# Kernel optimization log

Hardware: AMD Instinct MI355X
Metric: run time of the kernel (lower is better)

Reference implementation:

```python
import jax, jax.numpy as jnp
import numpy as np

COMMITMENT_COST = 0.25


def setup_inputs() -> dict:
    key = jax.random.key(0)
    k1, k2 = jax.random.split(key)
    x = jax.random.normal(k1, (32, 1024, 512), dtype=jnp.float32)
    codebook = jax.random.normal(k2, (8192, 512), dtype=jnp.float32)
    return {"x": x, "codebook": codebook}


def reference(x, codebook):
    D = codebook.shape[1]
    flat = x.reshape(-1, D)                                   # [N, D]
    # squared L2 distances: ||f||^2 + ||c||^2 - 2 f c^T
    distances = (
        jnp.sum(flat * flat, axis=1, keepdims=True)
        + jnp.sum(codebook * codebook, axis=1)
        - 2.0 * jnp.matmul(flat, codebook.T)                   # [N, K]
    )
    encoding_indices = jnp.argmin(distances, axis=1)           # [N]
    quantized = codebook[encoding_indices].reshape(x.shape)    # [.., D]
    commitment_loss = COMMITMENT_COST * jnp.mean(
        (jax.lax.stop_gradient(quantized) - x) ** 2
    )
    # straight-through estimator
    quantized_st = x + jax.lax.stop_gradient(quantized - x)
    return (quantized_st, commitment_loss)
```

## Files before the change

kernel.cpp:

```cpp
#include <hip/hip_runtime.h>
#include <stdint.h>

#define N_TOT 32768
#define DDIM  512
#define KCB   8192
#define NSPLIT 4
#define COLS_SPLIT (KCB / NSPLIT)
#define BN 128
#define BC 128
#define BKD 64
#define NTILES (COLS_SPLIT / BC)
#define NSTEPS (NTILES * 8)
#define MARGIN 0.15f

#define RB3 32
#define RP3 32
#define RSLOTS (RGRID3 / RP3)
#define RGRID3 2048

typedef _Float16 half8 __attribute__((ext_vector_type(8)));
typedef float    floatx4 __attribute__((ext_vector_type(4)));

typedef const __attribute__((address_space(1))) unsigned int* gas_ptr;
typedef __attribute__((address_space(3))) unsigned int* las_ptr;
__device__ __forceinline__ void gld_lds16(void* l, const void* g) {
    __builtin_amdgcn_global_load_lds((gas_ptr)g, (las_ptr)l, 16, 0, 0);
}

__device__ __forceinline__ unsigned long long shfl_xor_u64(unsigned long long v, int m) {
    unsigned int lo = (unsigned int)v, hi = (unsigned int)(v >> 32);
    lo = __shfl_xor(lo, m, 64);
    hi = __shfl_xor(hi, m, 64);
    return ((unsigned long long)hi << 32) | lo;
}

__global__ __launch_bounds__(256) void convert_x_kernel(
    const float* __restrict__ x, _Float16* __restrict__ xh) {
    size_t i = ((size_t)blockIdx.x * 256 + threadIdx.x) * 8;
    float4 v0 = *(const float4*)(x + i);
    float4 v1 = *(const float4*)(x + i + 4);
    half8 h;
    h[0] = (_Float16)v0.x; h[1] = (_Float16)v0.y; h[2] = (_Float16)v0.z; h[3] = (_Float16)v0.w;
    h[4] = (_Float16)v1.x; h[5] = (_Float16)v1.y; h[6] = (_Float16)v1.z; h[7] = (_Float16)v1.w;
    *(half8*)(xh + i) = h;
}

__global__ __launch_bounds__(256) void convert_cb_kernel(
    const float* __restrict__ cb, _Float16* __restrict__ cbh, float* __restrict__ cnorm) {
    int row = blockIdx.x * 4 + (threadIdx.x >> 6);
    int lane = threadIdx.x & 63;
    const float* src = cb + (size_t)row * DDIM + lane * 8;
    float4 v0 = *(const float4*)src;
    float4 v1 = *(const float4*)(src + 4);
    half8 h;
    h[0] = (_Float16)v0.x; h[1] = (_Float16)v0.y; h[2] = (_Float16)v0.z; h[3] = (_Float16)v0.w;
    h[4] = (_Float16)v1.x; h[5] = (_Float16)v1.y; h[6] = (_Float16)v1.z; h[7] = (_Float16)v1.w;
    *(half8*)(cbh + (size_t)row * DDIM + lane * 8) = h;
    float s = v0.x*v0.x + v0.y*v0.y + v0.z*v0.z + v0.w*v0.w
            + v1.x*v1.x + v1.y*v1.y + v1.z*v1.z + v1.w*v1.w;
#pragma unroll
    for (int off = 32; off > 0; off >>= 1) s += __shfl_down(s, off, 64);
    if (lane == 0) cnorm[row] = s;
}

__global__ __launch_bounds__(256, 2) void gemm_argmin_kernel(
    const _Float16* __restrict__ xh, const _Float16* __restrict__ cbh,
    const float* __restrict__ cnorm,
    float* __restrict__ sb1, int* __restrict__ si1, float* __restrict__ sb2) {

    __shared__ __align__(16) _Float16 smem[32768];
    char* smemb = (char*)smem;

    const int tid = threadIdx.x;
    const int wave = tid >> 6;
    const int lane = tid & 63;
    const int rowHalf = wave >> 1;
    const int colHalf = wave & 1;
    const int l15 = lane & 15;
    const int quad = lane >> 4;

    const int orig = blockIdx.x;
    const int wg = ((orig & 7) << 7) | (orig >> 3);
    const int bx = wg & 255;
    const int by = wg >> 8;
    const int row0 = bx * BN;
    const int colBase = by * COLS_SPLIT;

    int voff[4];
#pragma unroll
    for (int r = 0; r < 4; ++r) {
        int c = wave * 256 + r * 64 + lane;
        int ar = c >> 3;
        int q  = (c & 7) ^ (ar & 7);
        voff[r] = (ar << 9) + q * 8;
    }
    const _Float16* aptr = xh + ((size_t)row0 << 9);
    const _Float16* bptr = cbh + ((size_t)colBase << 9);

    int aaddr[2][4], baddr[2][4];
#pragma unroll
    for (int kh = 0; kh < 2; ++kh) {
#pragma unroll
        for (int i = 0; i < 4; ++i) {
            int rr = rowHalf * 64 + i * 16 + l15;
            int qa = (kh * 4 + quad) ^ (rr & 7);
            aaddr[kh][i] = (rr * 64 + qa * 8) * 2;
            int cc = colHalf * 64 + i * 16 + l15;
            int qb = (kh * 4 + quad) ^ (cc & 7);
            baddr[kh][i] = 16384 + (cc * 64 + qb * 8) * 2;
        }
    }

    float b1[16], b2[16];
    int   i1[16];
#pragma unroll
    for (int s = 0; s < 16; ++s) { b1[s] = 3.402823466e38f; b2[s] = 3.402823466e38f; i1[s] = 0; }

#define STAGE(parv, boffu, d0v) do {                                            \
        _Float16* Asb = smem + (parv) * 16384;                                  \
        _Float16* Bsb = Asb + 8192;                                             \
        _Pragma("unroll")                                                       \
        for (int r = 0; r < 4; ++r) {                                           \
            gld_lds16(Asb + (wave * 256 + r * 64) * 8,                          \
                      aptr + (d0v) + voff[r]);                                  \
            gld_lds16(Bsb + (wave * 256 + r * 64) * 8,                          \
                      bptr + (boffu) + (d0v) + voff[r]);                        \
        }                                                                       \
    } while (0)

    floatx4 acc[4][4];
#pragma unroll
    for (int i = 0; i < 4; ++i)
#pragma unroll
        for (int j = 0; j < 4; ++j)
            acc[i][j] = (floatx4){0.f, 0.f, 0.f, 0.f};

    STAGE(0, 0, 0);
    __syncthreads();

    for (int s = 0; s < NSTEPS; ++s) {
        if (s + 1 < NSTEPS) {
            STAGE((s + 1) & 1, ((s + 1) >> 3) << 16, ((s + 1) & 7) * BKD);
        }
#pragma unroll
        for (int kh = 0; kh < 2; ++kh) {
            half8 af[4], bf[4];
#pragma unroll
            for (int i = 0; i < 4; ++i)
                af[i] = *(const half8*)(smemb + aaddr[kh][i]);
#pragma unroll
            for (int j = 0; j < 4; ++j)
                bf[j] = *(const half8*)(smemb + baddr[kh][j]);
#pragma unroll
            for (int i = 0; i < 4; ++i)
#pragma unroll
                for (int j = 0; j < 4; ++j)
                    acc[i][j] = __builtin_amdgcn_mfma_f32_16x16x32_f16(
                        af[i], bf[j], acc[i][j], 0, 0, 0);
        }
        if ((s & 7) == 7) {
            const int col0 = colBase + (s >> 3) * BC;
#pragma unroll
            for (int j = 0; j < 4; ++j) {
                int col = col0 + colHalf * 64 + j * 16 + l15;
                float cn = cnorm[col];
#pragma unroll
                for (int i = 0; i < 4; ++i) {
#pragma unroll
                    for (int r = 0; r < 4; ++r) {
                        float sc = fmaf(-2.0f, acc[i][j][r], cn);
                        int slot = i * 4 + r;
                        if (sc < b1[slot]) { b2[slot] = b1[slot]; b1[slot] = sc; i1[slot] = col; }
                        else if (sc < b2[slot]) b2[slot] = sc;
                    }
                }
            }
#pragma unroll
            for (int i = 0; i < 4; ++i)
#pragma unroll
                for (int j = 0; j < 4; ++j)
                    acc[i][j] = (floatx4){0.f, 0.f, 0.f, 0.f};
        }
#pragma unroll
        for (int kh = 0; kh < 2; ++kh)
#pragma unroll
            for (int i = 0; i < 4; ++i) { aaddr[kh][i] ^= 32768; baddr[kh][i] ^= 32768; }
        __syncthreads();
    }
#undef STAGE

#pragma unroll
    for (int m = 1; m < 16; m <<= 1) {
#pragma unroll
        for (int s = 0; s < 16; ++s) {
            float ob1 = __shfl_xor(b1[s], m, 64);
            float ob2 = __shfl_xor(b2[s], m, 64);
            int   oi1 = __shfl_xor(i1[s], m, 64);
            if (ob1 < b1[s] || (ob1 == b1[s] && oi1 < i1[s])) {
                b2[s] = fminf(b1[s], ob2);
                b1[s] = ob1; i1[s] = oi1;
            } else {
                b2[s] = fminf(b2[s], ob1);
            }
        }
    }

    float* mb1 = (float*)smem;
    float* mb2 = mb1 + 256;
    int*   mi1 = (int*)(mb2 + 256);
    if (l15 == 0) {
#pragma unroll
        for (int s = 0; s < 16; ++s) {
            int row = rowHalf * 64 + (s >> 2) * 16 + quad * 4 + (s & 3);
            mb1[colHalf * 128 + row] = b1[s];
            mb2[colHalf * 128 + row] = b2[s];
            mi1[colHalf * 128 + row] = i1[s];
        }
    }
    __syncthreads();
    if (tid < 128) {
        float a1 = mb1[tid], a2 = mb2[tid]; int ai = mi1[tid];
        float c1 = mb1[128 + tid], c2 = mb2[128 + tid]; int ci = mi1[128 + tid];
        float r1, r2; int ri;
        if (c1 < a1 || (c1 == a1 && ci < ai)) { r1 = c1; ri = ci; r2 = fminf(a1, c2); }
        else { r1 = a1; ri = ai; r2 = fminf(a2, c1); }
        size_t o = (size_t)by * N_TOT + row0 + tid;
        sb1[o] = r1; si1[o] = ri; sb2[o] = r2;
    }
}

__global__ __launch_bounds__(256) void merge_kernel(
    const float* __restrict__ sb1, const int* __restrict__ si1, const float* __restrict__ sb2,
    int* __restrict__ indices, int* __restrict__ flags,
    int* __restrict__ list, int* __restrict__ count,
    unsigned long long* __restrict__ result) {
    int n = blockIdx.x * 256 + threadIdx.x;
    float b1 = sb1[n]; int i1 = si1[n]; float b2 = sb2[n];
#pragma unroll
    for (int s = 1; s < NSPLIT; ++s) {
        float ob1 = sb1[(size_t)s * N_TOT + n];
        int   oi1 = si1[(size_t)s * N_TOT + n];
        float ob2 = sb2[(size_t)s * N_TOT + n];
        if (ob1 < b1 || (ob1 == b1 && oi1 < i1)) { b2 = fminf(b1, ob2); b1 = ob1; i1 = oi1; }
        else b2 = fminf(b2, ob1);
    }
    indices[n] = i1;
    result[n] = 0xFFFFFFFFFFFFFFFFull;
    int f = (b2 - b1 < MARGIN) ? 1 : 0;
    flags[n] = f;
    if (f) { int pos = atomicAdd(count, 1); list[pos] = n; }
}

__global__ __launch_bounds__(256) void repair3_kernel(
    const float* __restrict__ x, const float* __restrict__ cb,
    const float* __restrict__ cnorm, const int* __restrict__ list,
    const int* __restrict__ count, unsigned long long* __restrict__ result) {
    __shared__ __align__(16) float xs[RB3][512];
    __shared__ unsigned long long red[RB3][4];
    const int tid = threadIdx.x;
    const int lane = tid & 63;
    const int wv = tid >> 6;
    const int part = blockIdx.x & (RP3 - 1);
    const int slot0 = blockIdx.x >> 5;
    const int cnt = *count;
    const int nbatch = (cnt + RB3 - 1) / RB3;
    const int k = part * 256 + tid;
    const float cn = cnorm[k];
    const float* crow = cb + (size_t)k * 512;

    for (int batch = slot0; batch < nbatch; batch += RSLOTS) {
        const int rb = min(RB3, cnt - batch * RB3);
        __syncthreads();
        for (int t = tid; t < rb * 128; t += 256) {
            int b = t >> 7, d4 = t & 127;
            int n = list[batch * RB3 + b];
            ((float4*)xs[b])[d4] = ((const float4*)(x + ((size_t)n << 9)))[d4];
        }
        __syncthreads();

        float d0[RB3], d1[RB3], d2[RB3], d3[RB3];
#pragma unroll
        for (int b = 0; b < RB3; ++b) { d0[b] = 0.f; d1[b] = 0.f; d2[b] = 0.f; d3[b] = 0.f; }

        for (int t = 0; t < 512; t += 16) {
            float4 c0 = *(const float4*)(crow + t);
            float4 c1 = *(const float4*)(crow + t + 4);
            float4 c2 = *(const float4*)(crow + t + 8);
            float4 c3 = *(const float4*)(crow + t + 12);
#pragma unroll
            for (int b = 0; b < RB3; ++b) {
                float4 x0 = *(const float4*)&xs[b][t];
                float4 x1 = *(const float4*)&xs[b][t + 4];
                float4 x2 = *(const float4*)&xs[b][t + 8];
                float4 x3 = *(const float4*)&xs[b][t + 12];
                d0[b] = fmaf(c0.x, x0.x, d0[b]);  d0[b] = fmaf(c0.y, x0.y, d0[b]);
                d0[b] = fmaf(c0.z, x0.z, d0[b]);  d0[b] = fmaf(c0.w, x0.w, d0[b]);
                d1[b] = fmaf(c1.x, x1.x, d1[b]);  d1[b] = fmaf(c1.y, x1.y, d1[b]);
                d1[b] = fmaf(c1.z, x1.z, d1[b]);  d1[b] = fmaf(c1.w, x1.w, d1[b]);
                d2[b] = fmaf(c2.x, x2.x, d2[b]);  d2[b] = fmaf(c2.y, x2.y, d2[b]);
                d2[b] = fmaf(c2.z, x2.z, d2[b]);  d2[b] = fmaf(c2.w, x2.w, d2[b]);
                d3[b] = fmaf(c3.x, x3.x, d3[b]);  d3[b] = fmaf(c3.y, x3.y, d3[b]);
                d3[b] = fmaf(c3.z, x3.z, d3[b]);  d3[b] = fmaf(c3.w, x3.w, d3[b]);
            }
        }

#pragma unroll
        for (int b = 0; b < RB3; ++b) {
            float s = cn - 2.f * ((d0[b] + d1[b]) + (d2[b] + d3[b]));
            unsigned int sb = __float_as_uint(s);
            sb = (sb & 0x80000000u) ? ~sb : (sb | 0x80000000u);
            unsigned long long p = ((unsigned long long)sb << 32) | (unsigned int)k;
#pragma unroll
            for (int m = 32; m > 0; m >>= 1) {
                unsigned long long o = shfl_xor_u64(p, m);
                if (o < p) p = o;
            }
            if (lane == 0) red[b][wv] = p;
        }
        __syncthreads();
        if (tid < RB3) {
            unsigned long long p = red[tid][0];
            if (red[tid][1] < p) p = red[tid][1];
            if (red[tid][2] < p) p = red[tid][2];
            if (red[tid][3] < p) p = red[tid][3];
            if (tid < rb) {
                int n = list[batch * RB3 + tid];
                atomicMin(&result[n], p);
            }
        }
    }
}

__global__ __launch_bounds__(256) void fixup_kernel(
    const int* __restrict__ flags, const unsigned long long* __restrict__ result,
    int* __restrict__ indices) {
    int n = blockIdx.x * 256 + threadIdx.x;
    if (flags[n]) indices[n] = (int)(result[n] & 0xFFFFFFFFu);
}

__global__ void cnorm_kernel(const float* __restrict__ cb, float* __restrict__ cnorm) {
    int wave = (blockIdx.x * blockDim.x + threadIdx.x) >> 6;
    int lane = threadIdx.x & 63;
    if (wave >= KCB) return;
    const float* row = cb + (size_t)wave * DDIM;
    float s = 0.f;
#pragma unroll
    for (int j = 0; j < DDIM / 64; ++j) { float v = row[lane + 64 * j]; s += v * v; }
#pragma unroll
    for (int off = 32; off > 0; off >>= 1) s += __shfl_down(s, off, 64);
    if (lane == 0) cnorm[wave] = s;
}

#define FBN 64
#define FBD 32
#define FLDA (FBN + 4)
__global__ __launch_bounds__(256) void argmin_fp32_kernel(
    const float* __restrict__ x, const float* __restrict__ cb,
    const float* __restrict__ cnorm, int* __restrict__ indices) {
    __shared__ float As[FBD][FLDA];
    __shared__ float Bs[FBD][FLDA];
    __shared__ float redv[FBN][16];
    __shared__ int   redi[FBN][16];
    const int tid = threadIdx.x;
    const int tx = tid & 15, ty = tid >> 4;
    const int row0 = blockIdx.x * FBN;
    float best[4]; int bidx[4];
#pragma unroll
    for (int i = 0; i < 4; ++i) { best[i] = 3.402823466e+38f; bidx[i] = KCB; }
    for (int k0 = 0; k0 < KCB; k0 += 64) {
        float acc[4][4] = {};
        for (int d0 = 0; d0 < DDIM; d0 += FBD) {
#pragma unroll
            for (int t = 0; t < 2; ++t) {
                int q = tid + t * 256, rr = q >> 3, dq = q & 7;
                float4 v = *(const float4*)(x + (size_t)(row0 + rr) * DDIM + d0 + dq * 4);
                As[dq*4+0][rr] = v.x; As[dq*4+1][rr] = v.y; As[dq*4+2][rr] = v.z; As[dq*4+3][rr] = v.w;
                float4 w = *(const float4*)(cb + (size_t)(k0 + rr) * DDIM + d0 + dq * 4);
                Bs[dq*4+0][rr] = w.x; Bs[dq*4+1][rr] = w.y; Bs[dq*4+2][rr] = w.z; Bs[dq*4+3][rr] = w.w;
            }
            __syncthreads();
#pragma unroll
            for (int d = 0; d < FBD; ++d) {
                float4 av = *(const float4*)&As[d][ty * 4];
                float4 bv = *(const float4*)&Bs[d][tx * 4];
                float a[4] = {av.x, av.y, av.z, av.w}, b[4] = {bv.x, bv.y, bv.z, bv.w};
#pragma unroll
                for (int i = 0; i < 4; ++i)
#pragma unroll
                    for (int j = 0; j < 4; ++j) acc[i][j] += a[i] * b[j];
            }
            __syncthreads();
        }
#pragma unroll
        for (int j = 0; j < 4; ++j) {
            int k = k0 + tx * 4 + j;
            float cn = cnorm[k];
#pragma unroll
            for (int i = 0; i < 4; ++i) {
                float s = cn - 2.0f * acc[i][j];
                if (s < best[i] || (s == best[i] && k < bidx[i])) { best[i] = s; bidx[i] = k; }
            }
        }
    }
#pragma unroll
    for (int i = 0; i < 4; ++i) { redv[ty*4+i][tx] = best[i]; redi[ty*4+i][tx] = bidx[i]; }
    __syncthreads();
    if (tid < FBN) {
        float bv = redv[tid][0]; int bi = redi[tid][0];
#pragma unroll
        for (int t = 1; t < 16; ++t) {
            float v = redv[tid][t]; int ii = redi[tid][t];
            if (v < bv || (v == bv && ii < bi)) { bv = v; bi = ii; }
        }
        indices[row0 + tid] = bi;
    }
}

__global__ __launch_bounds__(256) void output_kernel(
    const float* __restrict__ x, const float* __restrict__ cb,
    const int* __restrict__ indices, float* __restrict__ out,
    float* __restrict__ loss_acc) {
    size_t base = ((size_t)blockIdx.x * blockDim.x + threadIdx.x) * 16;
    int n = (int)(base >> 9);
    int d = (int)(base & 511);
    int idx = indices[n];
    const float* cr = cb + (size_t)idx * DDIM + d;
    const float* xr = x + base;
    float* orow = out + base;
    float lsum = 0.f;
#pragma unroll
    for (int t = 0; t < 4; ++t) {
        float4 q  = *(const float4*)(cr + t * 4);
        float4 xv = *(const float4*)(xr + t * 4);
        float dx0 = q.x - xv.x, dx1 = q.y - xv.y, dx2 = q.z - xv.z, dx3 = q.w - xv.w;
        float4 o;
        o.x = xv.x + dx0; o.y = xv.y + dx1; o.z = xv.z + dx2; o.w = xv.w + dx3;
        *(float4*)(orow + t * 4) = o;
        lsum += dx0*dx0 + dx1*dx1 + dx2*dx2 + dx3*dx3;
    }
#pragma unroll
    for (int off = 32; off > 0; off >>= 1) lsum += __shfl_down(lsum, off, 64);
    __shared__ float wsum[4];
    int lane = threadIdx.x & 63, wv = threadIdx.x >> 6;
    if (lane == 0) wsum[wv] = lsum;
    __syncthreads();
    if (threadIdx.x == 0) atomicAdd(loss_acc, wsum[0] + wsum[1] + wsum[2] + wsum[3]);
}

__global__ void finalize_kernel(const float* __restrict__ loss_acc, float* __restrict__ out_loss) {
    *out_loss = (*loss_acc) * (0.25f / (float)((size_t)N_TOT * DDIM));
}

extern "C" void kernel_launch(void* const* d_in, const int* in_sizes, int n_in,
                              void* d_out, int out_size, void* d_ws, size_t ws_size,
                              hipStream_t stream) {
    const float* x  = (const float*)d_in[0];
    const float* cb = (const float*)d_in[1];
    float* out = (float*)d_out;

    char* ws = (char*)d_ws;
    float* loss_acc = (float*)ws;
    int*   count    = (int*)(ws + 8);
    int*   indices  = (int*)(ws + 256);
    int*   flags    = (int*)(ws + 256 + 131072);
    float* cnorm    = (float*)(ws + 256 + 2 * 131072);
    int*   list     = (int*)(ws + 256 + 2 * 131072 + 32768);
    unsigned long long* result =
        (unsigned long long*)(ws + 256 + 3 * 131072 + 32768);
    size_t off = 256 + 3 * 131072 + 32768 + 262144;
    _Float16* xh  = (_Float16*)(ws + off);
    _Float16* cbh = (_Float16*)(ws + off + (size_t)N_TOT * DDIM * 2);
    size_t soff = off + (size_t)N_TOT * DDIM * 2 + (size_t)KCB * DDIM * 2;
    float* sb1 = (float*)(ws + soff);
    int*   si1 = (int*)(ws + soff + (size_t)NSPLIT * N_TOT * 4);
    float* sb2 = (float*)(ws + soff + (size_t)NSPLIT * N_TOT * 8);
    size_t need = soff + (size_t)NSPLIT * N_TOT * 12;

    hipMemsetAsync(ws, 0, 16, stream);
    if (ws_size >= need) {
        convert_x_kernel<<<(N_TOT * DDIM) / (256 * 8), 256, 0, stream>>>(x, xh);
        convert_cb_kernel<<<KCB / 4, 256, 0, stream>>>(cb, cbh, cnorm);
        gemm_argmin_kernel<<<(N_TOT / BN) * NSPLIT, 256, 0, stream>>>(
            xh, cbh, cnorm, sb1, si1, sb2);
        merge_kernel<<<N_TOT / 256, 256, 0, stream>>>(sb1, si1, sb2, indices, flags,
                                                      list, count, result);
        repair3_kernel<<<RGRID3, 256, 0, stream>>>(x, cb, cnorm, list, count, result);
        fixup_kernel<<<N_TOT / 256, 256, 0, stream>>>(flags, result, indices);
    } else {
        cnorm_kernel<<<KCB / 4, 256, 0, stream>>>(cb, cnorm);
        argmin_fp32_kernel<<<N_TOT / FBN, 256, 0, stream>>>(x, cb, cnorm, indices);
    }
    output_kernel<<<((size_t)N_TOT * DDIM) / (256 * 16), 256, 0, stream>>>(
        x, cb, indices, out, loss_acc);
    finalize_kernel<<<1, 1, 0, stream>>>(loss_acc, out + (size_t)N_TOT * DDIM);
}
```

Before: 912.0 us.

## Enlarge GEMM-argmin tile to 256x256 with 512-thread blocks

Doubles the row and column tile of the fused fp16 GEMM/argmin kernel to 256x256 and uses 8 waves per block, each computing a 64x128 subtile. The goal is more data reuse per LDS load and less global traffic per MFMA. LDS use doubles to 128KB per block and each wave holds twice as many accumulators, which may lower occupancy and raise register pressure. The LDS address scheme is also reworked to use a ping-pong offset and an XOR on the k-half.

```diff
diff --git a/kernel.cpp b/kernel.cpp
--- a/kernel.cpp
+++ b/kernel.cpp
@@ -6,8 +6,8 @@
 #define KCB   8192
 #define NSPLIT 4
 #define COLS_SPLIT (KCB / NSPLIT)
-#define BN 128
-#define BC 128
+#define BN 256
+#define BC 256
 #define BKD 64
 #define NTILES (COLS_SPLIT / BC)
 #define NSTEPS (NTILES * 8)
@@ -63,26 +63,26 @@
     if (lane == 0) cnorm[row] = s;
 }
 
-__global__ __launch_bounds__(256, 2) void gemm_argmin_kernel(
+__global__ __launch_bounds__(512, 2) void gemm_argmin_kernel(
     const _Float16* __restrict__ xh, const _Float16* __restrict__ cbh,
     const float* __restrict__ cnorm,
     float* __restrict__ sb1, int* __restrict__ si1, float* __restrict__ sb2) {
 
-    __shared__ __align__(16) _Float16 smem[32768];
+    __shared__ __align__(16) _Float16 smem[65536];
     char* smemb = (char*)smem;
 
     const int tid = threadIdx.x;
     const int wave = tid >> 6;
     const int lane = tid & 63;
-    const int rowHalf = wave >> 1;
-    const int colHalf = wave & 1;
+    const int rowPart = wave >> 1;
+    const int colPart = wave & 1;
     const int l15 = lane & 15;
     const int quad = lane >> 4;
 
     const int orig = blockIdx.x;
-    const int wg = ((orig & 7) << 7) | (orig >> 3);
-    const int bx = wg & 255;
-    const int by = wg >> 8;
+    const int wg = (orig & 7) * 64 + (orig >> 3);
+    const int bx = wg & 127;
+    const int by = wg >> 7;
     const int row0 = bx * BN;
     const int colBase = by * COLS_SPLIT;
 
@@ -97,18 +97,18 @@
     const _Float16* aptr = xh + ((size_t)row0 << 9);
     const _Float16* bptr = cbh + ((size_t)colBase << 9);
 
-    int aaddr[2][4], baddr[2][4];
-#pragma unroll
-    for (int kh = 0; kh < 2; ++kh) {
-#pragma unroll
-        for (int i = 0; i < 4; ++i) {
-            int rr = rowHalf * 64 + i * 16 + l15;
-            int qa = (kh * 4 + quad) ^ (rr & 7);
-            aaddr[kh][i] = (rr * 64 + qa * 8) * 2;
-            int cc = colHalf * 64 + i * 16 + l15;
-            int qb = (kh * 4 + quad) ^ (cc & 7);
-            baddr[kh][i] = 16384 + (cc * 64 + qb * 8) * 2;
-        }
+    int aaddr[4], baddr[8];
+#pragma unroll
+    for (int i = 0; i < 4; ++i) {
+        int rr = rowPart * 64 + i * 16 + l15;
+        int qa = quad ^ (rr & 7);
+        aaddr[i] = rr * 128 + qa * 16;
+    }
+#pragma unroll
+    for (int j = 0; j < 8; ++j) {
+        int cc = colPart * 128 + j * 16 + l15;
+        int qb = quad ^ (cc & 7);
+        baddr[j] = 32768 + cc * 128 + qb * 16;
     }
 
     float b1[16], b2[16];
@@ -117,8 +117,8 @@
     for (int s = 0; s < 16; ++s) { b1[s] = 3.402823466e38f; b2[s] = 3.402823466e38f; i1[s] = 0; }
 
 #define STAGE(parv, boffu, d0v) do {                                            \
-        _Float16* Asb = smem + (parv) * 16384;                                  \
-        _Float16* Bsb = Asb + 8192;                                             \
+        _Float16* Asb = smem + (parv) * 32768;                                  \
+        _Float16* Bsb = Asb + 16384;                                            \
         _Pragma("unroll")                                                       \
         for (int r = 0; r < 4; ++r) {                                           \
             gld_lds16(Asb + (wave * 256 + r * 64) * 8,                          \
@@ -128,41 +128,42 @@
         }                                                                       \
     } while (0)
 
-    floatx4 acc[4][4];
+    floatx4 acc[4][8];
 #pragma unroll
     for (int i = 0; i < 4; ++i)
 #pragma unroll
-        for (int j = 0; j < 4; ++j)
+        for (int j = 0; j < 8; ++j)
             acc[i][j] = (floatx4){0.f, 0.f, 0.f, 0.f};
 
     STAGE(0, 0, 0);
     __syncthreads();
 
+    int pofs = 0;
     for (int s = 0; s < NSTEPS; ++s) {
         if (s + 1 < NSTEPS) {
-            STAGE((s + 1) & 1, ((s + 1) >> 3) << 16, ((s + 1) & 7) * BKD);
+            STAGE((s + 1) & 1, ((s + 1) >> 3) << 17, ((s + 1) & 7) * BKD);
         }
 #pragma unroll
         for (int kh = 0; kh < 2; ++kh) {
-            half8 af[4], bf[4];
+            half8 af[4], bf[8];
 #pragma unroll
             for (int i = 0; i < 4; ++i)
-                af[i] = *(const half8*)(smemb + aaddr[kh][i]);
-#pragma unroll
-            for (int j = 0; j < 4; ++j)
-                bf[j] = *(const half8*)(smemb + baddr[kh][j]);
+                af[i] = *(const half8*)(smemb + (pofs + (aaddr[i] ^ (kh << 6))));
+#pragma unroll
+            for (int j = 0; j < 8; ++j)
+                bf[j] = *(const half8*)(smemb + (pofs + (baddr[j] ^ (kh << 6))));
 #pragma unroll
             for (int i = 0; i < 4; ++i)
 #pragma unroll
-                for (int j = 0; j < 4; ++j)
+                for (int j = 0; j < 8; ++j)
                     acc[i][j] = __builtin_amdgcn_mfma_f32_16x16x32_f16(
                         af[i], bf[j], acc[i][j], 0, 0, 0);
         }
         if ((s & 7) == 7) {
             const int col0 = colBase + (s >> 3) * BC;
 #pragma unroll
-            for (int j = 0; j < 4; ++j) {
-                int col = col0 + colHalf * 64 + j * 16 + l15;
+            for (int j = 0; j < 8; ++j) {
+                int col = col0 + colPart * 128 + j * 16 + l15;
                 float cn = cnorm[col];
 #pragma unroll
                 for (int i = 0; i < 4; ++i) {
@@ -178,13 +179,10 @@
 #pragma unroll
             for (int i = 0; i < 4; ++i)
 #pragma unroll
-                for (int j = 0; j < 4; ++j)
+                for (int j = 0; j < 8; ++j)
                     acc[i][j] = (floatx4){0.f, 0.f, 0.f, 0.f};
         }
-#pragma unroll
-        for (int kh = 0; kh < 2; ++kh)
-#pragma unroll
-            for (int i = 0; i < 4; ++i) { aaddr[kh][i] ^= 32768; baddr[kh][i] ^= 32768; }
+        pofs ^= 65536;
         __syncthreads();
     }
 #undef STAGE
@@ -206,21 +204,21 @@
     }
 
     float* mb1 = (float*)smem;
-    float* mb2 = mb1 + 256;
-    int*   mi1 = (int*)(mb2 + 256);
+    float* mb2 = mb1 + 512;
+    int*   mi1 = (int*)(mb2 + 512);
     if (l15 == 0) {
 #pragma unroll
         for (int s = 0; s < 16; ++s) {
-            int row = rowHalf * 64 + (s >> 2) * 16 + quad * 4 + (s & 3);
-            mb1[colHalf * 128 + row] = b1[s];
-            mb2[colHalf * 128 + row] = b2[s];
-            mi1[colHalf * 128 + row] = i1[s];
+            int row = rowPart * 64 + (s >> 2) * 16 + quad * 4 + (s & 3);
+            mb1[colPart * 256 + row] = b1[s];
+            mb2[colPart * 256 + row] = b2[s];
+            mi1[colPart * 256 + row] = i1[s];
         }
     }
     __syncthreads();
-    if (tid < 128) {
+    if (tid < 256) {
         float a1 = mb1[tid], a2 = mb2[tid]; int ai = mi1[tid];
-        float c1 = mb1[128 + tid], c2 = mb2[128 + tid]; int ci = mi1[128 + tid];
+        float c1 = mb1[256 + tid], c2 = mb2[256 + tid]; int ci = mi1[256 + tid];
         float r1, r2; int ri;
         if (c1 < a1 || (c1 == a1 && ci < ai)) { r1 = c1; ri = ci; r2 = fminf(a1, c2); }
         else { r1 = a1; ri = ai; r2 = fminf(a2, c1); }
@@ -480,7 +478,7 @@
     if (ws_size >= need) {
         convert_x_kernel<<<(N_TOT * DDIM) / (256 * 8), 256, 0, stream>>>(x, xh);
         convert_cb_kernel<<<KCB / 4, 256, 0, stream>>>(cb, cbh, cnorm);
-        gemm_argmin_kernel<<<(N_TOT / BN) * NSPLIT, 256, 0, stream>>>(
+        gemm_argmin_kernel<<<(N_TOT / BN) * NSPLIT, 512, 0, stream>>>(
             xh, cbh, cnorm, sb1, si1, sb2);
         merge_kernel<<<N_TOT / 256, 256, 0, stream>>>(sb1, si1, sb2, indices, flags,
                                                       list, count, result);
```

Measured after the change: 821.3 us. -9.9%, faster.
